# Kernel optimization log

Hardware: AMD Instinct MI355X
Metric: run time of the kernel (lower is better)

## Reference

```python
import jax, jax.numpy as jnp
import numpy as np

# Constants mirroring the torch module / argparse defaults
DECAY = 0.2           # LIF membrane decay
DECAY_TRACE = 0.99    # pre-synaptic trace decay
DECAY_TRACE2 = 0.99   # post-synaptic trace decay
INH = 1.625           # lateral inhibition strength (mode='max')
A1 = 0.96             # STDP potentiation coefficient
A2 = 0.53             # STDP depression coefficient
PLUS = 0.002          # adaptive threshold increment
THR_CAP = 350.0       # threshold cap in getthresh
B, IN, OUT = 128, 8192, 4096


def setup_inputs() -> dict:
    key = jax.random.key(0)
    ks = jax.random.split(key, 7)
    x = (jax.random.uniform(ks[0], (B, IN)) < 0.1).astype(jnp.float32)
    # weight after normweight(): clamp to [0,1], scale each row so row-max == 0.1
    w = jax.random.uniform(ks[1], (OUT, IN))
    w = jnp.clip(w, 0.0, 1.0)
    w = w / (w.max(axis=1, keepdims=True) / 0.1)
    mem = jax.random.uniform(ks[2], (B, OUT)) * 10.0          # warm membrane state
    threshold = 20.0 + 40.0 * jax.random.uniform(ks[3], (OUT,))  # per-neuron adaptive threshold
    trace = jax.random.uniform(ks[4], (B, IN))                 # warm pre-trace
    trace2 = jax.random.uniform(ks[5], (B, OUT))               # warm post-trace
    wta_rand = jax.random.uniform(ks[6], (B, OUT))             # WTA random tie-breaker
    return {"x": x, "weight": w, "mem": mem, "threshold": threshold,
            "trace": trace, "trace2": trace2, "wta_rand": wta_rand,
            "time_window": 10}


def reference(x, weight, mem, threshold, trace, trace2, wta_rand, time_window):
    batch = x.shape[0]
    # linear (no bias): i = x @ W^T   [B, OUT]
    i = x @ weight.T
    # --- LIF membrane update with hard reset ---
    mem = mem * DECAY + i
    s = (mem >= threshold[None, :]).astype(x.dtype)
    mem = mem * (1.0 - s)
    # --- winner-take-all (k=1) with random tie-break among spiking neurons ---
    pos = s * wta_rand
    winner = s * (pos >= pos.max(axis=1, keepdims=True)).astype(x.dtype)
    # --- adaptive lateral inhibition (mode='max'): suppress losers' membrane ---
    any_spk = winner.max(axis=1, keepdims=True)  # rows that fired
    mem = mem - INH * i.max(axis=1, keepdims=True) * (1.0 - winner) * any_spk
    spikes = winner
    # --- STDP traces and weight updates (training path) ---
    trace2_dec = trace2 * DECAY_TRACE2               # trace2 BEFORE adding current spikes
    dw2 = jnp.einsum('bo,bi->oi', trace2_dec, x)     # post-pre depression term
    trace_new = trace * DECAY_TRACE + x              # pre-trace replaces x for dw
    dw = jnp.einsum('bo,bi->oi', spikes, trace_new)  # pre-post potentiation term
    # --- adaptive threshold balance (ATB) ---
    thr = threshold + PLUS * (i * spikes).sum(0)
    thr = thr - jnp.maximum(thr.max() - THR_CAP, 0.0)
    # accumulated STDP weight change self.dw
    dw_total = (A1 * dw - A2 * dw2) / (time_window * batch)
    return spikes, dw_total, thr, mem
```

## Files before the change

kernel.cpp:

```cpp
#include <hip/hip_runtime.h>
#include <hip/hip_bf16.h>

typedef unsigned short u16;
typedef __bf16 bf16x8 __attribute__((ext_vector_type(8)));
typedef u16   u16x4  __attribute__((ext_vector_type(4)));
typedef float f32x4  __attribute__((ext_vector_type(4)));

#define MFMA16(A,B,C) __builtin_amdgcn_mfma_f32_16x16x32_bf16(A,B,C,0,0,0)

#define B_DIM   128
#define IN_DIM  8192
#define OUT_DIM 4096

__device__ __forceinline__ u16 f2bf(float f){
  __hip_bfloat16 h = __float2bfloat16(f);
  return __builtin_bit_cast(u16, h);
}
__device__ __forceinline__ float bf2f(u16 u){
  __hip_bfloat16 h = __builtin_bit_cast(__hip_bfloat16, u);
  return __bfloat162float(h);
}

__global__ __launch_bounds__(256) void p0a(const float* __restrict__ x,
    const float* __restrict__ trace, u16* __restrict__ xbf,
    u16* __restrict__ Bcat){
  __shared__ u16 sx[64*130];
  __shared__ u16 st[64*130];
  const int in0 = blockIdx.x*64;
  const int tid = threadIdx.x;
  for (int rep=0; rep<32; ++rep){
    int flat = rep*256 + tid;
    int b = flat >> 6, ino = flat & 63;
    size_t gi = (size_t)b*IN_DIM + in0 + ino;
    float xv = x[gi];
    float tv = trace[gi];
    u16 xb = f2bf(xv);
    xbf[gi] = xb;
    sx[ino*130 + b] = xb;
    st[ino*130 + b] = f2bf(__fadd_rn(__fmul_rn(0.99f, tv), xv));
  }
  __syncthreads();
  for (int rep=0; rep<32; ++rep){
    int flat = rep*256 + tid;
    int row = flat >> 7, bc = flat & 127;
    size_t base = (size_t)(in0+row)*256;
    Bcat[base + bc]       = st[row*130 + bc];
    Bcat[base + 128 + bc] = sx[row*130 + bc];
  }
}

__global__ __launch_bounds__(256) void p_t128(const float* __restrict__ src,
    u16* __restrict__ Acat, const int* __restrict__ twp, float coef,
    int kofs, int* __restrict__ gmax){
  __shared__ u16 st[64*130];
  const int o0 = blockIdx.x*64;
  const int tid = threadIdx.x;
  if (gmax != nullptr && blockIdx.x==0 && tid==0) *gmax = 0;
  const float scale = coef / (float)(twp[0]*B_DIM);
  for (int rep=0; rep<32; ++rep){
    int flat = rep*256 + tid;
    int b = flat >> 6, oo = flat & 63;
    float v = src[(size_t)b*OUT_DIM + o0 + oo];
    st[oo*130 + b] = f2bf(v*scale);
  }
  __syncthreads();
  for (int rep=0; rep<32; ++rep){
    int flat = rep*256 + tid;
    int row = flat >> 7, bc = flat & 127;
    Acat[(size_t)(o0+row)*256 + kofs + bc] = st[row*130 + bc];
  }
}

__global__ __launch_bounds__(256) void k1_gemm(const float* __restrict__ W,
    const u16* __restrict__ xbf, float* __restrict__ part){
  __shared__ __align__(16) u16 whi[64*72];
  __shared__ __align__(16) u16 wlo[64*72];
  const int n0    = blockIdx.x*64;
  const int kc    = blockIdx.y;
  const int kbase = kc*1024;
  const int tid   = threadIdx.x;
  const int lane  = tid & 63, wid = tid >> 6;
  const int m0    = wid*32;
  const int l15   = lane & 15, lg = lane >> 4;

  f32x4 acc[2][4];
  #pragma unroll
  for (int a=0;a<2;++a)
    #pragma unroll
    for (int c=0;c<4;++c){ acc[a][c][0]=0.f; acc[a][c][1]=0.f; acc[a][c][2]=0.f; acc[a][c][3]=0.f; }

  for (int step=0; step<16; ++step){
    const int k0 = kbase + step*64;
    __syncthreads();
    #pragma unroll
    for (int j=0;j<4;++j){
      int q  = tid + 256*j;
      int r  = q >> 4;
      int c4 = (q & 15)*4;
      const float4 wv = *reinterpret_cast<const float4*>(
          &W[(size_t)(n0+r)*IN_DIM + k0 + c4]);
      float comp[4] = {wv.x, wv.y, wv.z, wv.w};
      u16 h[4], l[4];
      #pragma unroll
      for (int e=0;e<4;++e){
        u16 hh = f2bf(comp[e]);
        h[e] = hh;
        l[e] = f2bf(__fsub_rn(comp[e], bf2f(hh)));
      }
      *reinterpret_cast<u16x4*>(&whi[r*72 + c4]) = (u16x4){h[0],h[1],h[2],h[3]};
      *reinterpret_cast<u16x4*>(&wlo[r*72 + c4]) = (u16x4){l[0],l[1],l[2],l[3]};
    }
    __syncthreads();

    bf16x8 af[2][2];
    #pragma unroll
    for (int mi=0;mi<2;++mi)
      #pragma unroll
      for (int ks=0;ks<2;++ks)
        af[mi][ks] = *reinterpret_cast<const bf16x8*>(
            &xbf[(size_t)(m0 + 16*mi + l15)*IN_DIM + k0 + ks*32 + 8*lg]);

    #pragma unroll
    for (int ni=0;ni<4;++ni){
      const int bb = (16*ni + l15)*72 + 8*lg;
      #pragma unroll
      for (int ks=0;ks<2;++ks){
        bf16x8 bh = *reinterpret_cast<const bf16x8*>(&whi[bb + ks*32]);
        bf16x8 bl = *reinterpret_cast<const bf16x8*>(&wlo[bb + ks*32]);
        acc[0][ni] = MFMA16(af[0][ks], bh, acc[0][ni]);
        acc[1][ni] = MFMA16(af[1][ks], bh, acc[1][ni]);
        acc[0][ni] = MFMA16(af[0][ks], bl, acc[0][ni]);
        acc[1][ni] = MFMA16(af[1][ks], bl, acc[1][ni]);
      }
    }
  }
  #pragma unroll
  for (int mi=0;mi<2;++mi)
    #pragma unroll
    for (int ni=0;ni<4;++ni)
      #pragma unroll
      for (int r=0;r<4;++r){
        int row = m0 + 16*mi + 4*lg + r;
        int col = n0 + 16*ni + l15;
        part[((size_t)kc*B_DIM + row)*OUT_DIM + col] = acc[mi][ni][r];
      }
}

__global__ __launch_bounds__(256) void r1(const float* __restrict__ part,
    float* __restrict__ iacc){
  int idx = blockIdx.x*256 + threadIdx.x;
  float a = part[idx];
  #pragma unroll
  for (int c=1;c<8;++c) a = __fadd_rn(a, part[(size_t)c*524288 + idx]);
  iacc[idx] = a;
}

__global__ __launch_bounds__(256) void k2_lif(const float* __restrict__ iacc,
    const float* __restrict__ mem, const float* __restrict__ thr,
    const float* __restrict__ wta, float* __restrict__ spikes,
    float* __restrict__ mem_out){
  const int b = blockIdx.x;
  const int tid = threadIdx.x;
  const size_t base = (size_t)b*OUT_DIM;
  float vv[16], pv[16];
  int sm = 0;
  float pmax = -1.f, imax = -3.4e38f;
  #pragma unroll
  for (int j=0;j<16;++j){
    int o = tid + 256*j;
    float ii = iacc[base+o];
    float v  = __fadd_rn(__fmul_rn(mem[base+o], 0.2f), ii);
    bool  s  = (v >= thr[o]);
    float p  = s ? wta[base+o] : 0.f;
    vv[j]=v; pv[j]=p;
    sm |= s ? (1<<j) : 0;
    pmax = fmaxf(pmax, p);
    imax = fmaxf(imax, ii);
  }
  float anyv = (sm!=0) ? 1.f : 0.f;
  #pragma unroll
  for (int off=32; off>=1; off>>=1){
    pmax = fmaxf(pmax, __shfl_xor(pmax, off));
    imax = fmaxf(imax, __shfl_xor(imax, off));
    anyv = fmaxf(anyv, __shfl_xor(anyv, off));
  }
  __shared__ float sp[4], si[4], sa[4];
  int wid = tid>>6, lane = tid&63;
  if (lane==0){ sp[wid]=pmax; si[wid]=imax; sa[wid]=anyv; }
  __syncthreads();
  pmax = fmaxf(fmaxf(sp[0],sp[1]), fmaxf(sp[2],sp[3]));
  imax = fmaxf(fmaxf(si[0],si[1]), fmaxf(si[2],si[3]));
  anyv = fmaxf(fmaxf(sa[0],sa[1]), fmaxf(sa[2],sa[3]));
  float isub = __fmul_rn(1.625f, imax);
  #pragma unroll
  for (int j=0;j<16;++j){
    int o = tid + 256*j;
    bool s   = (sm>>j)&1;
    bool win = s && (pv[j] >= pmax);
    spikes[base+o] = win ? 1.f : 0.f;
    float mv  = s ? 0.f : vv[j];
    float sub = (anyv>0.f && !win) ? isub : 0.f;
    mem_out[base+o] = __fsub_rn(mv, sub);
  }
}

__global__ __launch_bounds__(256) void k3a(const float* __restrict__ iacc,
    const float* __restrict__ spikes, const float* __restrict__ threshold,
    float* __restrict__ thr0, int* __restrict__ gmax){
  const int o = blockIdx.x*256 + threadIdx.x;
  float acc = 0.f;
  for (int b=0;b<B_DIM;++b)
    acc = __fadd_rn(acc, __fmul_rn(iacc[(size_t)b*OUT_DIM+o], spikes[(size_t)b*OUT_DIM+o]));
  float t = __fadd_rn(threshold[o], __fmul_rn(0.002f, acc));
  thr0[o] = t;
  float m = t;
  #pragma unroll
  for (int off=32; off>=1; off>>=1) m = fmaxf(m, __shfl_xor(m, off));
  __shared__ float sm4[4];
  if ((threadIdx.x&63)==0) sm4[threadIdx.x>>6] = m;
  __syncthreads();
  if (threadIdx.x==0){
    m = fmaxf(fmaxf(sm4[0],sm4[1]), fmaxf(sm4[2],sm4[3]));
    atomicMax(gmax, __float_as_int(m));
  }
}

__global__ __launch_bounds__(256) void k3b(const float* __restrict__ thr0,
    const int* __restrict__ gmax, float* __restrict__ thr_out){
  int o = blockIdx.x*256 + threadIdx.x;
  float g  = __int_as_float(*gmax);
  float ex = fmaxf(__fsub_rn(g, 350.f), 0.f);
  thr_out[o] = __fsub_rn(thr0[o], ex);
}

__global__ __launch_bounds__(256) void k4_dw(const u16* __restrict__ Acat,
    const u16* __restrict__ Bcat, float* __restrict__ dw){
  const int it = blockIdx.x;
  const int ot = blockIdx.y;
  const int tid = threadIdx.x;
  const int lane = tid&63, wid = tid>>6;
  const int l15 = lane&15, lg = lane>>4;
  const int o0 = ot*64;
  const int iw = it*256 + wid*64;
  f32x4 acc[4][4];
  #pragma unroll
  for (int a=0;a<4;++a)
    #pragma unroll
    for (int c=0;c<4;++c){ acc[a][c][0]=0.f; acc[a][c][1]=0.f; acc[a][c][2]=0.f; acc[a][c][3]=0.f; }

  const size_t abase = (size_t)(o0 + l15)*256 + 8*lg;
  const size_t bbase = (size_t)(iw + l15)*256 + 8*lg;
  #pragma unroll
  for (int ks=0; ks<8; ++ks){
    const int k = ks*32;
    bf16x8 a[4], bb[4];
    #pragma unroll
    for (int mi=0;mi<4;++mi)
      a[mi] = *reinterpret_cast<const bf16x8*>(&Acat[abase + (size_t)mi*16*256 + k]);
    #pragma unroll
    for (int ni=0;ni<4;++ni)
      bb[ni] = *reinterpret_cast<const bf16x8*>(&Bcat[bbase + (size_t)ni*16*256 + k]);
    #pragma unroll
    for (int mi=0;mi<4;++mi)
      #pragma unroll
      for (int ni=0;ni<4;++ni)
        acc[mi][ni] = MFMA16(a[mi], bb[ni], acc[mi][ni]);
  }
  #pragma unroll
  for (int mi=0;mi<4;++mi)
    #pragma unroll
    for (int ni=0;ni<4;++ni)
      #pragma unroll
      for (int r=0;r<4;++r)
        dw[(size_t)(o0 + 16*mi + 4*lg + r)*IN_DIM + iw + 16*ni + l15] = acc[mi][ni][r];
}

extern "C" void kernel_launch(void* const* d_in, const int* in_sizes, int n_in,
                              void* d_out, int out_size, void* d_ws, size_t ws_size,
                              hipStream_t stream) {
  (void)in_sizes; (void)n_in; (void)out_size; (void)ws_size;
  const float* x      = (const float*)d_in[0];
  const float* weight = (const float*)d_in[1];
  const float* mem    = (const float*)d_in[2];
  const float* thresh = (const float*)d_in[3];
  const float* trace  = (const float*)d_in[4];
  const float* trace2 = (const float*)d_in[5];
  const float* wta    = (const float*)d_in[6];
  const int*   twp    = (const int*)d_in[7];

  float* out    = (float*)d_out;
  float* spikes = out;
  float* dwout  = out + 524288;
  float* throut = out + 34078720;
  float* memout = out + 34082816;

  char* ws = (char*)d_ws;
  float* iacc = (float*)ws;
  u16*   xbf  = (u16*)(ws + (2u<<20));
  u16*   Acat = (u16*)(ws + (4u<<20));
  u16*   Bcat = (u16*)(ws + (6u<<20));
  float* thr0 = (float*)(ws + (10u<<20));
  int*   gmax = (int*)(ws + (10u<<20) + 16384);

  float* part = dwout;

  p0a<<<dim3(128), dim3(256), 0, stream>>>(x, trace, xbf, Bcat);
  p_t128<<<dim3(64), dim3(256), 0, stream>>>(trace2, Acat, twp, -(0.53f*0.99f), 128, gmax);
  k1_gemm<<<dim3(64,8), dim3(256), 0, stream>>>(weight, xbf, part);
  r1<<<dim3(2048), dim3(256), 0, stream>>>(part, iacc);
  k2_lif<<<dim3(128), dim3(256), 0, stream>>>(iacc, mem, thresh, wta, spikes, memout);
  p_t128<<<dim3(64), dim3(256), 0, stream>>>(spikes, Acat, twp, 0.96f, 0, (int*)nullptr);
  k3a<<<dim3(16), dim3(256), 0, stream>>>(iacc, spikes, thresh, thr0, gmax);
  k3b<<<dim3(16), dim3(256), 0, stream>>>(thr0, gmax, throut);
  k4_dw<<<dim3(32,64), dim3(256), 0, stream>>>(Acat, Bcat, dwout);
}
```

Before: 367.7 us.

## Fuse prep kernels, register-prefetch GEMM weights, merge reduction into LIF, split threshold sum

```diff
diff --git a/kernel.cpp b/kernel.cpp
--- a/kernel.cpp
+++ b/kernel.cpp
@@ -21,61 +21,90 @@
   return __bfloat162float(h);
 }
 
-__global__ __launch_bounds__(256) void p0a(const float* __restrict__ x,
-    const float* __restrict__ trace, u16* __restrict__ xbf,
-    u16* __restrict__ Bcat){
-  __shared__ u16 sx[64*130];
-  __shared__ u16 st[64*130];
-  const int in0 = blockIdx.x*64;
-  const int tid = threadIdx.x;
-  for (int rep=0; rep<32; ++rep){
+__global__ __launch_bounds__(256) void prep(const float* __restrict__ x,
+    const float* __restrict__ trace, const float* __restrict__ trace2,
+    const int* __restrict__ twp, u16* __restrict__ xbf,
+    u16* __restrict__ Bcat, u16* __restrict__ Acat){
+  __shared__ u16 s0[64*130];
+  __shared__ u16 s1[64*130];
+  const int tid = threadIdx.x;
+  if (blockIdx.x < 128){
+    const int in0 = blockIdx.x*64;
+    #pragma unroll
+    for (int rep=0; rep<8; ++rep){
+      int flat = rep*256 + tid;
+      int b = flat >> 4, i4 = (flat & 15)*4;
+      size_t gi = (size_t)b*IN_DIM + in0 + i4;
+      float4 xv = *reinterpret_cast<const float4*>(&x[gi]);
+      float4 tv = *reinterpret_cast<const float4*>(&trace[gi]);
+      u16 xb[4];
+      #pragma unroll
+      for (int e=0;e<4;++e){
+        float xe = (&xv.x)[e];
+        xb[e] = f2bf(xe);
+        s0[(i4+e)*130 + b] = xb[e];
+        s1[(i4+e)*130 + b] = f2bf(__fadd_rn(__fmul_rn(0.99f, (&tv.x)[e]), xe));
+      }
+      *reinterpret_cast<u16x4*>(&xbf[gi]) = (u16x4){xb[0],xb[1],xb[2],xb[3]};
+    }
+    __syncthreads();
+    #pragma unroll
+    for (int rep=0; rep<32; ++rep){
+      int flat = rep*256 + tid;
+      int row = flat >> 7, bc = flat & 127;
+      size_t base = (size_t)(in0+row)*256;
+      Bcat[base + bc]       = s1[row*130 + bc];
+      Bcat[base + 128 + bc] = s0[row*130 + bc];
+    }
+  } else {
+    const int o0 = (blockIdx.x - 128)*64;
+    const float scale = -(0.53f*0.99f) / (float)(twp[0]*B_DIM);
+    #pragma unroll
+    for (int rep=0; rep<8; ++rep){
+      int flat = rep*256 + tid;
+      int b = flat >> 4, o4 = (flat & 15)*4;
+      float4 v = *reinterpret_cast<const float4*>(&trace2[(size_t)b*OUT_DIM + o0 + o4]);
+      #pragma unroll
+      for (int e=0;e<4;++e) s0[(o4+e)*130 + b] = f2bf((&v.x)[e]*scale);
+    }
+    __syncthreads();
+    #pragma unroll
+    for (int rep=0; rep<32; ++rep){
+      int flat = rep*256 + tid;
+      int row = flat >> 7, bc = flat & 127;
+      Acat[(size_t)(o0+row)*256 + 128 + bc] = s0[row*130 + bc];
+    }
+  }
+}
+
+__global__ __launch_bounds__(256) void t128s(const float* __restrict__ spikes,
+    const int* __restrict__ twp, u16* __restrict__ Acat){
+  __shared__ u16 s0[64*130];
+  const int o0 = blockIdx.x*64;
+  const int tid = threadIdx.x;
+  const float scale = 0.96f / (float)(twp[0]*B_DIM);
+  #pragma unroll
+  for (int rep=0; rep<8; ++rep){
     int flat = rep*256 + tid;
-    int b = flat >> 6, ino = flat & 63;
-    size_t gi = (size_t)b*IN_DIM + in0 + ino;
-    float xv = x[gi];
-    float tv = trace[gi];
-    u16 xb = f2bf(xv);
-    xbf[gi] = xb;
-    sx[ino*130 + b] = xb;
-    st[ino*130 + b] = f2bf(__fadd_rn(__fmul_rn(0.99f, tv), xv));
+    int b = flat >> 4, o4 = (flat & 15)*4;
+    float4 v = *reinterpret_cast<const float4*>(&spikes[(size_t)b*OUT_DIM + o0 + o4]);
+    #pragma unroll
+    for (int e=0;e<4;++e) s0[(o4+e)*130 + b] = f2bf((&v.x)[e]*scale);
   }
   __syncthreads();
+  #pragma unroll
   for (int rep=0; rep<32; ++rep){
     int flat = rep*256 + tid;
     int row = flat >> 7, bc = flat & 127;
-    size_t base = (size_t)(in0+row)*256;
-    Bcat[base + bc]       = st[row*130 + bc];
-    Bcat[base + 128 + bc] = sx[row*130 + bc];
-  }
-}
-
-__global__ __launch_bounds__(256) void p_t128(const float* __restrict__ src,
-    u16* __restrict__ Acat, const int* __restrict__ twp, float coef,
-    int kofs, int* __restrict__ gmax){
-  __shared__ u16 st[64*130];
-  const int o0 = blockIdx.x*64;
-  const int tid = threadIdx.x;
-  if (gmax != nullptr && blockIdx.x==0 && tid==0) *gmax = 0;
-  const float scale = coef / (float)(twp[0]*B_DIM);
-  for (int rep=0; rep<32; ++rep){
-    int flat = rep*256 + tid;
-    int b = flat >> 6, oo = flat & 63;
-    float v = src[(size_t)b*OUT_DIM + o0 + oo];
-    st[oo*130 + b] = f2bf(v*scale);
-  }
-  __syncthreads();
-  for (int rep=0; rep<32; ++rep){
-    int flat = rep*256 + tid;
-    int row = flat >> 7, bc = flat & 127;
-    Acat[(size_t)(o0+row)*256 + kofs + bc] = st[row*130 + bc];
+    Acat[(size_t)(o0+row)*256 + bc] = s0[row*130 + bc];
   }
 }
 
 __global__ __launch_bounds__(256) void k1_gemm(const float* __restrict__ W,
     const u16* __restrict__ xbf, float* __restrict__ part){
-  __shared__ __align__(16) u16 whi[64*72];
-  __shared__ __align__(16) u16 wlo[64*72];
-  const int n0    = blockIdx.x*64;
+  __shared__ __align__(16) u16 whi[32*72];
+  __shared__ __align__(16) u16 wlo[32*72];
+  const int n0    = blockIdx.x*32;
   const int kc    = blockIdx.y;
   const int kbase = kc*1024;
   const int tid   = threadIdx.x;
@@ -83,32 +112,40 @@
   const int m0    = wid*32;
   const int l15   = lane & 15, lg = lane >> 4;
 
-  f32x4 acc[2][4];
+  f32x4 acc[2][2];
   #pragma unroll
   for (int a=0;a<2;++a)
     #pragma unroll
-    for (int c=0;c<4;++c){ acc[a][c][0]=0.f; acc[a][c][1]=0.f; acc[a][c][2]=0.f; acc[a][c][3]=0.f; }
+    for (int c=0;c<2;++c){ acc[a][c][0]=0.f; acc[a][c][1]=0.f; acc[a][c][2]=0.f; acc[a][c][3]=0.f; }
+
+  const int qr[2] = { (tid)>>4, (tid+256)>>4 };
+  const int qc[2] = { (tid&15)*4, (tid&15)*4 };
+  float4 wreg[2];
+  #pragma unroll
+  for (int j=0;j<2;++j)
+    wreg[j] = *reinterpret_cast<const float4*>(
+        &W[(size_t)(n0+qr[j])*IN_DIM + kbase + qc[j]]);
 
   for (int step=0; step<16; ++step){
     const int k0 = kbase + step*64;
-    __syncthreads();
-    #pragma unroll
-    for (int j=0;j<4;++j){
-      int q  = tid + 256*j;
-      int r  = q >> 4;
-      int c4 = (q & 15)*4;
-      const float4 wv = *reinterpret_cast<const float4*>(
-          &W[(size_t)(n0+r)*IN_DIM + k0 + c4]);
-      float comp[4] = {wv.x, wv.y, wv.z, wv.w};
+    #pragma unroll
+    for (int j=0;j<2;++j){
       u16 h[4], l[4];
       #pragma unroll
       for (int e=0;e<4;++e){
-        u16 hh = f2bf(comp[e]);
+        float c = (&wreg[j].x)[e];
+        u16 hh = f2bf(c);
         h[e] = hh;
-        l[e] = f2bf(__fsub_rn(comp[e], bf2f(hh)));
+        l[e] = f2bf(__fsub_rn(c, bf2f(hh)));
       }
-      *reinterpret_cast<u16x4*>(&whi[r*72 + c4]) = (u16x4){h[0],h[1],h[2],h[3]};
-      *reinterpret_cast<u16x4*>(&wlo[r*72 + c4]) = (u16x4){l[0],l[1],l[2],l[3]};
+      *reinterpret_cast<u16x4*>(&whi[qr[j]*72 + qc[j]]) = (u16x4){h[0],h[1],h[2],h[3]};
+      *reinterpret_cast<u16x4*>(&wlo[qr[j]*72 + qc[j]]) = (u16x4){l[0],l[1],l[2],l[3]};
+    }
+    if (step < 15){
+      #pragma unroll
+      for (int j=0;j<2;++j)
+        wreg[j] = *reinterpret_cast<const float4*>(
+            &W[(size_t)(n0+qr[j])*IN_DIM + k0 + 64 + qc[j]]);
     }
     __syncthreads();
 
@@ -121,7 +158,7 @@
             &xbf[(size_t)(m0 + 16*mi + l15)*IN_DIM + k0 + ks*32 + 8*lg]);
 
     #pragma unroll
-    for (int ni=0;ni<4;++ni){
+    for (int ni=0;ni<2;++ni){
       const int bb = (16*ni + l15)*72 + 8*lg;
       #pragma unroll
       for (int ks=0;ks<2;++ks){
@@ -133,11 +170,12 @@
         acc[1][ni] = MFMA16(af[1][ks], bl, acc[1][ni]);
       }
     }
+    __syncthreads();
   }
   #pragma unroll
   for (int mi=0;mi<2;++mi)
     #pragma unroll
-    for (int ni=0;ni<4;++ni)
+    for (int ni=0;ni<2;++ni)
       #pragma unroll
       for (int r=0;r<4;++r){
         int row = m0 + 16*mi + 4*lg + r;
@@ -146,37 +184,45 @@
       }
 }
 
-__global__ __launch_bounds__(256) void r1(const float* __restrict__ part,
-    float* __restrict__ iacc){
-  int idx = blockIdx.x*256 + threadIdx.x;
-  float a = part[idx];
-  #pragma unroll
-  for (int c=1;c<8;++c) a = __fadd_rn(a, part[(size_t)c*524288 + idx]);
-  iacc[idx] = a;
-}
-
-__global__ __launch_bounds__(256) void k2_lif(const float* __restrict__ iacc,
+__global__ __launch_bounds__(512) void k2_lif(const float* __restrict__ part,
     const float* __restrict__ mem, const float* __restrict__ thr,
     const float* __restrict__ wta, float* __restrict__ spikes,
-    float* __restrict__ mem_out){
+    float* __restrict__ mem_out, float* __restrict__ iacc){
   const int b = blockIdx.x;
   const int tid = threadIdx.x;
   const size_t base = (size_t)b*OUT_DIM;
-  float vv[16], pv[16];
+  float vv[8], pv[8], ia[8];
   int sm = 0;
   float pmax = -1.f, imax = -3.4e38f;
   #pragma unroll
-  for (int j=0;j<16;++j){
-    int o = tid + 256*j;
-    float ii = iacc[base+o];
-    float v  = __fadd_rn(__fmul_rn(mem[base+o], 0.2f), ii);
-    bool  s  = (v >= thr[o]);
-    float p  = s ? wta[base+o] : 0.f;
-    vv[j]=v; pv[j]=p;
-    sm |= s ? (1<<j) : 0;
-    pmax = fmaxf(pmax, p);
-    imax = fmaxf(imax, ii);
-  }
+  for (int j=0;j<2;++j){
+    const int o = 4*tid + 2048*j;
+    f32x4 a = *reinterpret_cast<const f32x4*>(&part[base + o]);
+    #pragma unroll
+    for (int c=1;c<8;++c){
+      f32x4 p4 = *reinterpret_cast<const f32x4*>(
+          &part[((size_t)c*B_DIM + b)*OUT_DIM + o]);
+      #pragma unroll
+      for (int e=0;e<4;++e) a[e] = __fadd_rn(a[e], p4[e]);
+    }
+    *reinterpret_cast<f32x4*>(&iacc[base + o]) = a;
+    f32x4 m4 = *reinterpret_cast<const f32x4*>(&mem[base + o]);
+    f32x4 t4 = *reinterpret_cast<const f32x4*>(&thr[o]);
+    f32x4 w4 = *reinterpret_cast<const f32x4*>(&wta[base + o]);
+    #pragma unroll
+    for (int e=0;e<4;++e){
+      int idx = 4*j + e;
+      float ii = a[e];
+      float v  = __fadd_rn(__fmul_rn(m4[e], 0.2f), ii);
+      bool  s  = (v >= t4[e]);
+      float p  = s ? w4[e] : 0.f;
+      ia[idx]=ii; vv[idx]=v; pv[idx]=p;
+      sm |= s ? (1<<idx) : 0;
+      pmax = fmaxf(pmax, p);
+      imax = fmaxf(imax, ii);
+    }
+  }
+  (void)ia;
   float anyv = (sm!=0) ? 1.f : 0.f;
   #pragma unroll
   for (int off=32; off>=1; off>>=1){
@@ -184,59 +230,84 @@
     imax = fmaxf(imax, __shfl_xor(imax, off));
     anyv = fmaxf(anyv, __shfl_xor(anyv, off));
   }
-  __shared__ float sp[4], si[4], sa[4];
-  int wid = tid>>6, lane = tid&63;
+  __shared__ float sp[8], si[8], sa[8];
+  const int wid = tid>>6, lane = tid&63;
   if (lane==0){ sp[wid]=pmax; si[wid]=imax; sa[wid]=anyv; }
   __syncthreads();
-  pmax = fmaxf(fmaxf(sp[0],sp[1]), fmaxf(sp[2],sp[3]));
-  imax = fmaxf(fmaxf(si[0],si[1]), fmaxf(si[2],si[3]));
-  anyv = fmaxf(fmaxf(sa[0],sa[1]), fmaxf(sa[2],sa[3]));
-  float isub = __fmul_rn(1.625f, imax);
-  #pragma unroll
-  for (int j=0;j<16;++j){
-    int o = tid + 256*j;
-    bool s   = (sm>>j)&1;
-    bool win = s && (pv[j] >= pmax);
-    spikes[base+o] = win ? 1.f : 0.f;
-    float mv  = s ? 0.f : vv[j];
-    float sub = (anyv>0.f && !win) ? isub : 0.f;
-    mem_out[base+o] = __fsub_rn(mv, sub);
+  pmax = sp[0]; imax = si[0]; anyv = sa[0];
+  #pragma unroll
+  for (int k=1;k<8;++k){
+    pmax = fmaxf(pmax, sp[k]); imax = fmaxf(imax, si[k]); anyv = fmaxf(anyv, sa[k]);
+  }
+  const float isub = __fmul_rn(1.625f, imax);
+  #pragma unroll
+  for (int j=0;j<2;++j){
+    const int o = 4*tid + 2048*j;
+    f32x4 sp4, mm4;
+    #pragma unroll
+    for (int e=0;e<4;++e){
+      int idx = 4*j + e;
+      bool s   = (sm>>idx)&1;
+      bool win = s && (pv[idx] >= pmax);
+      sp4[e] = win ? 1.f : 0.f;
+      float mv  = s ? 0.f : vv[idx];
+      float sub = (anyv>0.f && !win) ? isub : 0.f;
+      mm4[e] = __fsub_rn(mv, sub);
+    }
+    *reinterpret_cast<f32x4*>(&spikes[base + o])  = sp4;
+    *reinterpret_cast<f32x4*>(&mem_out[base + o]) = mm4;
   }
 }
 
 __global__ __launch_bounds__(256) void k3a(const float* __restrict__ iacc,
-    const float* __restrict__ spikes, const float* __restrict__ threshold,
-    float* __restrict__ thr0, int* __restrict__ gmax){
-  const int o = blockIdx.x*256 + threadIdx.x;
+    const float* __restrict__ spikes, float* __restrict__ thrpart){
+  const int o  = blockIdx.x*256 + threadIdx.x;
+  const int bc = blockIdx.y;
   float acc = 0.f;
-  for (int b=0;b<B_DIM;++b)
+  #pragma unroll
+  for (int bb=0; bb<16; ++bb){
+    int b = bc*16 + bb;
     acc = __fadd_rn(acc, __fmul_rn(iacc[(size_t)b*OUT_DIM+o], spikes[(size_t)b*OUT_DIM+o]));
-  float t = __fadd_rn(threshold[o], __fmul_rn(0.002f, acc));
-  thr0[o] = t;
-  float m = t;
+  }
+  thrpart[(size_t)bc*OUT_DIM + o] = acc;
+}
+
+__global__ __launch_bounds__(1024) void k3bc(const float* __restrict__ thrpart,
+    const float* __restrict__ threshold, float* __restrict__ thr_out){
+  const int tid = threadIdx.x;
+  const int o = tid*4;
+  f32x4 s = *reinterpret_cast<const f32x4*>(&thrpart[o]);
+  #pragma unroll
+  for (int c=1;c<8;++c){
+    f32x4 p4 = *reinterpret_cast<const f32x4*>(&thrpart[(size_t)c*OUT_DIM + o]);
+    #pragma unroll
+    for (int e=0;e<4;++e) s[e] = __fadd_rn(s[e], p4[e]);
+  }
+  f32x4 t4 = *reinterpret_cast<const f32x4*>(&threshold[o]);
+  float t0[4];
+  #pragma unroll
+  for (int e=0;e<4;++e) t0[e] = __fadd_rn(t4[e], __fmul_rn(0.002f, s[e]));
+  float m = fmaxf(fmaxf(t0[0],t0[1]), fmaxf(t0[2],t0[3]));
   #pragma unroll
   for (int off=32; off>=1; off>>=1) m = fmaxf(m, __shfl_xor(m, off));
-  __shared__ float sm4[4];
-  if ((threadIdx.x&63)==0) sm4[threadIdx.x>>6] = m;
+  __shared__ float sm16[16];
+  const int wid = tid>>6, lane = tid&63;
+  if (lane==0) sm16[wid] = m;
   __syncthreads();
-  if (threadIdx.x==0){
-    m = fmaxf(fmaxf(sm4[0],sm4[1]), fmaxf(sm4[2],sm4[3]));
-    atomicMax(gmax, __float_as_int(m));
-  }
-}
-
-__global__ __launch_bounds__(256) void k3b(const float* __restrict__ thr0,
-    const int* __restrict__ gmax, float* __restrict__ thr_out){
-  int o = blockIdx.x*256 + threadIdx.x;
-  float g  = __int_as_float(*gmax);
+  float g = sm16[0];
+  #pragma unroll
+  for (int k=1;k<16;++k) g = fmaxf(g, sm16[k]);
   float ex = fmaxf(__fsub_rn(g, 350.f), 0.f);
-  thr_out[o] = __fsub_rn(thr0[o], ex);
+  f32x4 outv;
+  #pragma unroll
+  for (int e=0;e<4;++e) outv[e] = __fsub_rn(t0[e], ex);
+  *reinterpret_cast<f32x4*>(&thr_out[o]) = outv;
 }
 
 __global__ __launch_bounds__(256) void k4_dw(const u16* __restrict__ Acat,
     const u16* __restrict__ Bcat, float* __restrict__ dw){
-  const int it = blockIdx.x;
-  const int ot = blockIdx.y;
+  const int ot = blockIdx.x;
+  const int it = blockIdx.y;
   const int tid = threadIdx.x;
   const int lane = tid&63, wid = tid>>6;
   const int l15 = lane&15, lg = lane>>4;
@@ -295,22 +366,19 @@
   float* memout = out + 34082816;
 
   char* ws = (char*)d_ws;
-  float* iacc = (float*)ws;
-  u16*   xbf  = (u16*)(ws + (2u<<20));
-  u16*   Acat = (u16*)(ws + (4u<<20));
-  u16*   Bcat = (u16*)(ws + (6u<<20));
-  float* thr0 = (float*)(ws + (10u<<20));
-  int*   gmax = (int*)(ws + (10u<<20) + 16384);
+  float* iacc    = (float*)ws;
+  u16*   xbf     = (u16*)(ws + (2u<<20));
+  u16*   Acat    = (u16*)(ws + (4u<<20));
+  u16*   Bcat    = (u16*)(ws + (6u<<20));
+  float* thrpart = (float*)(ws + (10u<<20));
 
   float* part = dwout;
 
-  p0a<<<dim3(128), dim3(256), 0, stream>>>(x, trace, xbf, Bcat);
-  p_t128<<<dim3(64), dim3(256), 0, stream>>>(trace2, Acat, twp, -(0.53f*0.99f), 128, gmax);
-  k1_gemm<<<dim3(64,8), dim3(256), 0, stream>>>(weight, xbf, part);
-  r1<<<dim3(2048), dim3(256), 0, stream>>>(part, iacc);
-  k2_lif<<<dim3(128), dim3(256), 0, stream>>>(iacc, mem, thresh, wta, spikes, memout);
-  p_t128<<<dim3(64), dim3(256), 0, stream>>>(spikes, Acat, twp, 0.96f, 0, (int*)nullptr);
-  k3a<<<dim3(16), dim3(256), 0, stream>>>(iacc, spikes, thresh, thr0, gmax);
-  k3b<<<dim3(16), dim3(256), 0, stream>>>(thr0, gmax, throut);
-  k4_dw<<<dim3(32,64), dim3(256), 0, stream>>>(Acat, Bcat, dwout);
-}
+  prep <<<dim3(192),    dim3(256),  0, stream>>>(x, trace, trace2, twp, xbf, Bcat, Acat);
+  k1_gemm<<<dim3(128,8),dim3(256),  0, stream>>>(weight, xbf, part);
+  k2_lif<<<dim3(128),   dim3(512),  0, stream>>>(part, mem, thresh, wta, spikes, memout, iacc);
+  t128s<<<dim3(64),     dim3(256),  0, stream>>>(spikes, twp, Acat);
+  k3a  <<<dim3(16,8),   dim3(256),  0, stream>>>(iacc, spikes, thrpart);
+  k3bc <<<dim3(1),      dim3(1024), 0, stream>>>(thrpart, thresh, throut);
+  k4_dw<<<dim3(64,32),  dim3(256),  0, stream>>>(Acat, Bcat, dwout);
+}
```

After: 357.9 us. 2.7% less time.
